# Kernel tuning notes

Measured on AMD Instinct MI355X. Metric: run time of the kernel, lower is better.

Reference implementation:

```python
import jax, jax.numpy as jnp
import numpy as np

E, S, G, H, O = 50000, 16, 64, 256, 16


def _mlp(x, W0, b0, W1, b1, W2, b2):
    # x: [..., 2] -> [..., out]
    x = jax.nn.relu(x @ W0 + b0)
    x = jax.nn.relu(x @ W1 + b1)
    return x @ W2 + b2


def setup_inputs() -> dict:
    key = jax.random.key(0)
    ks = jax.random.split(key, 9)
    ob = jax.random.normal(ks[0], (E, S, 3), dtype=jnp.float32)
    action = jax.random.randint(ks[1], (E, S), 0, O).astype(jnp.int64)
    graph_ids = jnp.sort(jax.random.randint(ks[2], (E,), 0, G)).astype(jnp.int32)
    def lin(k, fin, fout):
        return jax.random.normal(k, (fin, fout), dtype=jnp.float32) / jnp.sqrt(jnp.float32(fin))
    return {
        "ob": ob, "action": action, "graph_ids": graph_ids,
        "aW0": lin(ks[3], 2, H), "ab0": jnp.zeros((H,), jnp.float32),
        "aW1": lin(ks[4], H, H), "ab1": jnp.zeros((H,), jnp.float32),
        "aW2": lin(ks[5], H, O), "ab2": jnp.zeros((O,), jnp.float32),
        "cW0": lin(ks[6], 2, H), "cb0": jnp.zeros((H,), jnp.float32),
        "cW1": lin(ks[7], H, H), "cb1": jnp.zeros((H,), jnp.float32),
        "cW2": lin(ks[8], H, 1), "cb2": jnp.zeros((1,), jnp.float32),
    }


def reference(ob, action, graph_ids, aW0, ab0, aW1, ab1, aW2, ab2,
              cW0, cb0, cW1, cb1, cW2, cb2):
    num_edges = ob.shape[0]
    # edge_mask: torch `ob.select(2,0).long() == 0` (truncation toward zero)
    edge_mask = ob[..., 0].astype(jnp.int32) == 0            # [E,S] bool
    mf = edge_mask.astype(ob.dtype)                          # [E,S]
    h = ob[..., 1:3]                                         # [E,S,2]

    # Actor logits over all (edge,sample); mask replaces gather/scatter
    logits = _mlp(h, aW0, ab0, aW1, ab1, aW2, ab2)           # [E,S,O]
    logp = jax.nn.log_softmax(logits, axis=-1)               # [E,S,O]

    # log-prob of given actions, scattered to zeros outside the mask
    alp = jnp.take_along_axis(logp, action[..., None], axis=-1)[..., 0]
    action_log_probs = alp * mf                              # [E,S]

    # critic edge values, scattered to zeros outside the mask
    vals = _mlp(h, cW0, cb0, cW1, cb1, cW2, cb2)[..., 0] * mf  # [E,S]

    # entropy averaged over masked (subgraph) entries only
    ent = -jnp.sum(jnp.exp(logp) * logp, axis=-1)            # [E,S]
    avg_entropy = jnp.sum(ent * mf) / jnp.sum(mf)

    # sum_efeat: per-graph segment sum over edges, divided by num_edges
    value_preds = jax.ops.segment_sum(vals, graph_ids, num_segments=G) / num_edges  # [G,S]

    return action_log_probs, avg_entropy, value_preds, edge_mask
```

## Files before the change

### kernel.cpp

```cpp
#include <hip/hip_runtime.h>
#include <stdint.h>


typedef __attribute__((ext_vector_type(8))) short bf16x8;
typedef __attribute__((ext_vector_type(4))) float f32x4;
typedef __attribute__((ext_vector_type(4))) uint32_t u32x4;

#define NROWS    800000
#define NCHUNK   12500
#define OUT_ENT  800000
#define OUT_VP   800001
#define OUT_MASK 801025

#define SWZ(row) ((((row) & 7) << 4) ^ (((row) & 16) << 1))

__device__ __forceinline__ short f2bf(float x) {
  union { float f; uint32_t u; } v; v.f = x;
  return (short)(uint16_t)((v.u + 0x7FFFu + ((v.u >> 16) & 1u)) >> 16);
}
__device__ __forceinline__ float bf2f(short h) {
  union { uint32_t u; float f; } v; v.u = ((uint32_t)(uint16_t)h) << 16;
  return v.f;
}
template <int C>
__device__ __forceinline__ float dppf(float x) {
  int r = __builtin_amdgcn_update_dpp(0, __builtin_bit_cast(int, x), C, 0xF, 0xF, true);
  return __builtin_bit_cast(float, r);
}
__device__ __forceinline__ float red16_sum(float x) {
  x += dppf<0xB1>(x); x += dppf<0x4E>(x); x += dppf<0x124>(x); x += dppf<0x128>(x); return x;
}
__device__ __forceinline__ float red16_max(float x) {
  x = fmaxf(x, dppf<0xB1>(x)); x = fmaxf(x, dppf<0x4E>(x));
  x = fmaxf(x, dppf<0x124>(x)); x = fmaxf(x, dppf<0x128>(x)); return x;
}
__device__ __forceinline__ uint32_t cvt_pk_bf16(float a, float b) {
  uint32_t r; asm("v_cvt_pk_bf16_f32 %0, %1, %2" : "=v"(r) : "v"(a), "v"(b)); return r;
}

__global__ void zero_kernel(float* out, float* wsf) {
  int t = threadIdx.x + blockIdx.x * blockDim.x;
  for (int i = t; i < 1025; i += 1024) out[OUT_ENT + i] = 0.0f;
  if (t == 0) { wsf[0] = 0.0f; wsf[1] = 0.0f; }
}
__global__ void final_kernel(float* out, const float* wsf) {
  if (threadIdx.x == 0 && blockIdx.x == 0)
    out[OUT_ENT] = (wsf[1] > 0.0f) ? (wsf[0] / wsf[1]) : 0.0f;
}

#define A_ACT1 0
#define A_ACT2 32768
#define A_W2H  65536
#define A_W0   73728
#define A_B0   75776
#define A_OB   76800
#define A_SZ   78848

__global__ void __launch_bounds__(512, 2) ac_actor(
    const float* __restrict__ ob, const int* __restrict__ action,
    const float* __restrict__ aW0, const float* __restrict__ ab0,
    const float* __restrict__ aW1, const float* __restrict__ ab1,
    const float* __restrict__ aW2, const float* __restrict__ ab2,
    float* __restrict__ out, float* __restrict__ wsf)
{
  extern __shared__ char smem[];
  float* w0buf = (float*)(smem + A_W0);
  float* b0buf = (float*)(smem + A_B0);
  float* obufA = (float*)(smem + A_OB);
  const f32x4* w04 = (const f32x4*)(smem + A_W0);
  const f32x4* b04 = (const f32x4*)(smem + A_B0);
  __shared__ float went[8], wmf[8];

  const int tid = threadIdx.x, lane = tid & 63, wave = tid >> 6;
  const int l15 = lane & 15, l4 = lane >> 4;

  w0buf[tid] = aW0[tid];
  if (tid < 256) b0buf[tid] = ab0[tid];
  for (int id = tid; id < 4096; id += 512) {
    int n = id >> 8, k = id & 255;
    *(short*)(smem + A_W2H + n * 512 + ((k * 2) ^ SWZ(n))) = f2bf(aW2[k * 16 + n]);
  }
  const int colbase = wave * 32;
  float b1lane[2] = { ab1[colbase + l15], ab1[colbase + 16 + l15] };
  float b2lane = ab2[l15];
  bf16x8 bh[2][8];
  #pragma unroll
  for (int ct = 0; ct < 2; ++ct) {
    const int n = colbase + ct * 16 + l15;
    #pragma unroll
    for (int ks = 0; ks < 8; ++ks) {
      const int k0 = ks * 32 + 8 * l4;
      bf16x8 h8;
      #pragma unroll
      for (int j = 0; j < 8; ++j) h8[j] = f2bf(aW1[(k0 + j) * 256 + n]);
      bh[ct][ks] = h8;
    }
  }
  const int c0 = blockIdx.x, stride = gridDim.x;
  float sob = 0.0f;
  if (tid < 192) { obufA[tid] = ob[c0 * 192 + tid]; }
  { int cn = c0 + stride; if (cn < NCHUNK && tid < 192) sob = ob[cn * 192 + tid]; }
  __syncthreads();

  float entacc = 0.0f, mfacc = 0.0f;
  int buf = 0;
  for (int c = c0; c < NCHUNK; c += stride, buf ^= 1) {
    const int row0 = c * 64;
    const float* ocur = obufA + buf * 256;
    float* onxt = (float*)(obufA + (buf ^ 1) * 256);

    if (tid < 64) out[OUT_MASK + row0 + tid] = ((int)ocur[tid * 3] == 0) ? 1.0f : 0.0f;
    {
      const int kb = tid & 31;
      f32x4 wa0 = w04[kb * 2], wa1 = w04[kb * 2 + 1];
      f32x4 wb0 = w04[64 + kb * 2], wb1 = w04[64 + kb * 2 + 1];
      f32x4 ba0 = b04[kb * 2], ba1 = b04[kb * 2 + 1];
      #pragma unroll
      for (int i = 0; i < 4; ++i) {
        int row = wave * 2 + 16 * i + (lane >> 5);
        float h0 = ocur[row * 3 + 1], h1 = ocur[row * 3 + 2];
        f32x4 va, vb;
        #pragma unroll
        for (int j = 0; j < 4; ++j) {
          va[j] = fmaxf(fmaf(h0, wa0[j], fmaf(h1, wb0[j], ba0[j])), 0.0f);
          vb[j] = fmaxf(fmaf(h0, wa1[j], fmaf(h1, wb1[j], ba1[j])), 0.0f);
        }
        u32x4 v;
        v[0] = cvt_pk_bf16(va[0], va[1]);
        v[1] = cvt_pk_bf16(va[2], va[3]);
        v[2] = cvt_pk_bf16(vb[0], vb[1]);
        v[3] = cvt_pk_bf16(vb[2], vb[3]);
        *(u32x4*)(smem + A_ACT1 + row * 512 + ((kb * 16) ^ SWZ(row))) = v;
      }
    }
    if (tid < 192) onxt[tid] = sob;
    { int c2 = c + 2 * stride; if (c2 < NCHUNK && tid < 192) sob = ob[c2 * 192 + tid]; }
    __syncthreads();

    const bool evn = (l15 & 1) == 0;
    #pragma unroll 1
    for (int rtp = 0; rtp < 2; ++rtp) {
      f32x4 acc[2][2];
      #pragma unroll
      for (int h = 0; h < 2; ++h)
        #pragma unroll
        for (int ct = 0; ct < 2; ++ct) acc[h][ct] = (f32x4){0.f, 0.f, 0.f, 0.f};
      const int rA0 = rtp * 32 + l15, rA1 = rA0 + 16;
      #pragma unroll
      for (int ks = 0; ks < 8; ++ks) {
        const int cb = ks * 64 + 16 * l4;
        bf16x8 a0 = *(const bf16x8*)(smem + A_ACT1 + rA0 * 512 + (cb ^ SWZ(rA0)));
        bf16x8 a1 = *(const bf16x8*)(smem + A_ACT1 + rA1 * 512 + (cb ^ SWZ(rA1)));
        acc[0][0] = __builtin_amdgcn_mfma_f32_16x16x32_bf16(a0, bh[0][ks], acc[0][0], 0, 0, 0);
        acc[0][1] = __builtin_amdgcn_mfma_f32_16x16x32_bf16(a0, bh[1][ks], acc[0][1], 0, 0, 0);
        acc[1][0] = __builtin_amdgcn_mfma_f32_16x16x32_bf16(a1, bh[0][ks], acc[1][0], 0, 0, 0);
        acc[1][1] = __builtin_amdgcn_mfma_f32_16x16x32_bf16(a1, bh[1][ks], acc[1][1], 0, 0, 0);
      }
      #pragma unroll
      for (int ct = 0; ct < 2; ++ct) {
        const int colb = (colbase + ct * 16 + (l15 & ~1)) * 2;
        #pragma unroll
        for (int r = 0; r < 4; ++r) {
          float v0 = fmaxf(acc[0][ct][r] + b1lane[ct], 0.0f);
          float v1 = fmaxf(acc[1][ct][r] + b1lane[ct], 0.0f);
          float n0 = dppf<0xB1>(v0), n1 = dppf<0xB1>(v1);
          uint32_t w = cvt_pk_bf16(evn ? v0 : n1, evn ? n0 : v1);
          int rr = rtp * 32 + (evn ? 0 : 16) + 4 * l4 + r;
          *(uint32_t*)(smem + A_ACT2 + rr * 512 + (colb ^ SWZ(rr))) = w;
        }
      }
    }
    __syncthreads();

    if (wave < 4) {
      const int rowA = wave * 16 + l15;
      const int swA = SWZ(rowA), swW = SWZ(l15);
      f32x4 ae = {0.f,0.f,0.f,0.f}, ao = {0.f,0.f,0.f,0.f};
      #pragma unroll
      for (int ks = 0; ks < 8; ks += 2) {
        const int cb0 = ks * 64 + 16 * l4, cb1 = cb0 + 64;
        bf16x8 a0 = *(const bf16x8*)(smem + A_ACT2 + rowA * 512 + (cb0 ^ swA));
        bf16x8 a1 = *(const bf16x8*)(smem + A_ACT2 + rowA * 512 + (cb1 ^ swA));
        bf16x8 w0f = *(const bf16x8*)(smem + A_W2H + l15 * 512 + (cb0 ^ swW));
        bf16x8 w1f = *(const bf16x8*)(smem + A_W2H + l15 * 512 + (cb1 ^ swW));
        ae = __builtin_amdgcn_mfma_f32_16x16x32_bf16(a0, w0f, ae, 0, 0, 0);
        ao = __builtin_amdgcn_mfma_f32_16x16x32_bf16(a1, w1f, ao, 0, 0, 0);
      }
      #pragma unroll
      for (int r = 0; r < 4; ++r) {
        const int rl = wave * 16 + 4 * l4 + r;
        float x = ae[r] + ao[r] + b2lane;
        float m = red16_max(x);
        float e = __expf(x - m);
        float s = red16_sum(e);
        float t = red16_sum(e * (x - m));
        float ls = __logf(s);
        float mfr = ((int)ob[(row0 + rl) * 3] == 0) ? 1.0f : 0.0f;
        int av = action[row0 + rl];
        if (l15 == av) out[row0 + rl] = (x - m - ls) * mfr;
        if (l15 == 0) { entacc += (ls - t / s) * mfr; mfacc += mfr; }
      }
    }
  }
  #pragma unroll
  for (int d = 1; d < 64; d <<= 1) { entacc += __shfl_xor(entacc, d); mfacc += __shfl_xor(mfacc, d); }
  if (lane == 0) { went[wave] = entacc; wmf[wave] = mfacc; }
  __syncthreads();
  if (tid == 0) {
    float e = 0.f, m = 0.f;
    #pragma unroll
    for (int i = 0; i < 8; ++i) { e += went[i]; m += wmf[i]; }
    atomicAdd(&wsf[0], e); atomicAdd(&wsf[1], m);
  }
}

#define C_ACT1 0
#define C_ACT2 32768
#define C_W0   65536
#define C_B0   67584
#define C_W2F  68608
#define C_OB   69632
#define C_SZ   71680

__global__ void __launch_bounds__(512, 2) ac_critic(
    const float* __restrict__ ob, const int* __restrict__ graph_ids,
    const float* __restrict__ cW0, const float* __restrict__ cb0,
    const float* __restrict__ cW1, const float* __restrict__ cb1,
    const float* __restrict__ cW2, const float* __restrict__ cb2,
    float* __restrict__ out)
{
  extern __shared__ char smem[];
  float* w0buf = (float*)(smem + C_W0);
  float* b0buf = (float*)(smem + C_B0);
  float* w2buf = (float*)(smem + C_W2F);
  float* obufA = (float*)(smem + C_OB);
  const f32x4* w04 = (const f32x4*)(smem + C_W0);
  const f32x4* b04 = (const f32x4*)(smem + C_B0);
  const f32x4* w24 = (const f32x4*)(smem + C_W2F);

  const int tid = threadIdx.x, lane = tid & 63, wave = tid >> 6;
  const int l15 = lane & 15, l4 = lane >> 4;

  w0buf[tid] = cW0[tid];
  if (tid < 256) b0buf[tid] = cb0[tid];
  if (tid >= 256 && tid < 512) w2buf[tid - 256] = cW2[tid - 256];
  const float cb2v = cb2[0];
  const int colbase = wave * 32;
  float b1lane[2] = { cb1[colbase + l15], cb1[colbase + 16 + l15] };

  bf16x8 bh[2][8];
  #pragma unroll
  for (int ct = 0; ct < 2; ++ct) {
    const int n = colbase + ct * 16 + l15;
    #pragma unroll
    for (int ks = 0; ks < 8; ++ks) {
      const int k0 = ks * 32 + 8 * l4;
      bf16x8 h8;
      #pragma unroll
      for (int j = 0; j < 8; ++j) h8[j] = f2bf(cW1[(k0 + j) * 256 + n]);
      bh[ct][ks] = h8;
    }
  }
  const int c0 = blockIdx.x, stride = gridDim.x;
  float sob = 0.0f;
  if (tid < 192) { obufA[tid] = ob[c0 * 192 + tid]; }
  { int cn = c0 + stride; if (cn < NCHUNK && tid < 192) sob = ob[cn * 192 + tid]; }
  __syncthreads();

  int buf = 0;
  for (int c = c0; c < NCHUNK; c += stride, buf ^= 1) {
    const int row0 = c * 64;
    const float* ocur = obufA + buf * 256;
    float* onxt = (float*)(obufA + (buf ^ 1) * 256);

    {
      const int kb = tid & 31;
      f32x4 wa0 = w04[kb * 2], wa1 = w04[kb * 2 + 1];
      f32x4 wb0 = w04[64 + kb * 2], wb1 = w04[64 + kb * 2 + 1];
      f32x4 ba0 = b04[kb * 2], ba1 = b04[kb * 2 + 1];
      #pragma unroll
      for (int i = 0; i < 4; ++i) {
        int row = wave * 2 + 16 * i + (lane >> 5);
        float h0 = ocur[row * 3 + 1], h1 = ocur[row * 3 + 2];
        f32x4 va, vb;
        #pragma unroll
        for (int j = 0; j < 4; ++j) {
          va[j] = fmaxf(fmaf(h0, wa0[j], fmaf(h1, wb0[j], ba0[j])), 0.0f);
          vb[j] = fmaxf(fmaf(h0, wa1[j], fmaf(h1, wb1[j], ba1[j])), 0.0f);
        }
        u32x4 v;
        v[0] = cvt_pk_bf16(va[0], va[1]);
        v[1] = cvt_pk_bf16(va[2], va[3]);
        v[2] = cvt_pk_bf16(vb[0], vb[1]);
        v[3] = cvt_pk_bf16(vb[2], vb[3]);
        *(u32x4*)(smem + C_ACT1 + row * 512 + ((kb * 16) ^ SWZ(row))) = v;
      }
    }
    if (tid < 192) onxt[tid] = sob;
    { int c2 = c + 2 * stride; if (c2 < NCHUNK && tid < 192) sob = ob[c2 * 192 + tid]; }
    __syncthreads();

    const bool evn = (l15 & 1) == 0;
    #pragma unroll 1
    for (int rtp = 0; rtp < 2; ++rtp) {
      f32x4 acc[2][2];
      #pragma unroll
      for (int h = 0; h < 2; ++h)
        #pragma unroll
        for (int ct = 0; ct < 2; ++ct) acc[h][ct] = (f32x4){0.f, 0.f, 0.f, 0.f};
      const int rA0 = rtp * 32 + l15, rA1 = rA0 + 16;
      #pragma unroll
      for (int ks = 0; ks < 8; ++ks) {
        const int cb = ks * 64 + 16 * l4;
        bf16x8 a0 = *(const bf16x8*)(smem + C_ACT1 + rA0 * 512 + (cb ^ SWZ(rA0)));
        bf16x8 a1 = *(const bf16x8*)(smem + C_ACT1 + rA1 * 512 + (cb ^ SWZ(rA1)));
        acc[0][0] = __builtin_amdgcn_mfma_f32_16x16x32_bf16(a0, bh[0][ks], acc[0][0], 0, 0, 0);
        acc[0][1] = __builtin_amdgcn_mfma_f32_16x16x32_bf16(a0, bh[1][ks], acc[0][1], 0, 0, 0);
        acc[1][0] = __builtin_amdgcn_mfma_f32_16x16x32_bf16(a1, bh[0][ks], acc[1][0], 0, 0, 0);
        acc[1][1] = __builtin_amdgcn_mfma_f32_16x16x32_bf16(a1, bh[1][ks], acc[1][1], 0, 0, 0);
      }
      #pragma unroll
      for (int ct = 0; ct < 2; ++ct) {
        const int colb = (colbase + ct * 16 + (l15 & ~1)) * 2;
        #pragma unroll
        for (int r = 0; r < 4; ++r) {
          float v0 = fmaxf(acc[0][ct][r] + b1lane[ct], 0.0f);
          float v1 = fmaxf(acc[1][ct][r] + b1lane[ct], 0.0f);
          float n0 = dppf<0xB1>(v0), n1 = dppf<0xB1>(v1);
          uint32_t w = cvt_pk_bf16(evn ? v0 : n1, evn ? n0 : v1);
          int rr = rtp * 32 + (evn ? 0 : 16) + 4 * l4 + r;
          *(uint32_t*)(smem + C_ACT2 + rr * 512 + (colb ^ SWZ(rr))) = w;
        }
      }
    }
    __syncthreads();

    if (wave < 4) {
      const int rt = wave;
      const int row = rt * 16 + l15;
      const int sw = SWZ(row);
      float val = 0.0f;
      #pragma unroll
      for (int ks = 0; ks < 8; ++ks) {
        bf16x8 a = *(const bf16x8*)(smem + C_ACT2 + row * 512 + ((ks * 64 + 16 * l4) ^ sw));
        f32x4 wA = w24[ks * 8 + 2 * l4], wB = w24[ks * 8 + 2 * l4 + 1];
        #pragma unroll
        for (int j = 0; j < 4; ++j) {
          val = fmaf(bf2f(a[j]), wA[j], val);
          val = fmaf(bf2f(a[4 + j]), wB[j], val);
        }
      }
      val += __shfl_xor(val, 16);
      val += __shfl_xor(val, 32);
      if (l4 == 0) {
        float o0 = ob[(row0 + row) * 3];
        if ((int)o0 == 0) {
          int g = graph_ids[c * 4 + rt];
          atomicAdd(&out[OUT_VP + g * 16 + l15], (val + cb2v) * (1.0f / 50000.0f));
        }
      }
    }
  }
}

extern "C" void kernel_launch(void* const* d_in, const int* in_sizes, int n_in,
                              void* d_out, int out_size, void* d_ws, size_t ws_size,
                              hipStream_t stream) {
  const float* ob     = (const float*)d_in[0];
  const int*   action = (const int*)d_in[1];
  const int*   gids   = (const int*)d_in[2];
  const float* aW0 = (const float*)d_in[3],  *ab0 = (const float*)d_in[4];
  const float* aW1 = (const float*)d_in[5],  *ab1 = (const float*)d_in[6];
  const float* aW2 = (const float*)d_in[7],  *ab2 = (const float*)d_in[8];
  const float* cW0 = (const float*)d_in[9],  *cb0 = (const float*)d_in[10];
  const float* cW1 = (const float*)d_in[11], *cb1 = (const float*)d_in[12];
  const float* cW2 = (const float*)d_in[13], *cb2 = (const float*)d_in[14];
  float* out = (float*)d_out;
  float* wsf = (float*)d_ws;

  zero_kernel<<<2, 512, 0, stream>>>(out, wsf);
  ac_actor<<<512, 512, A_SZ, stream>>>(ob, action, aW0, ab0, aW1, ab1, aW2, ab2, out, wsf);
  ac_critic<<<512, 512, C_SZ, stream>>>(ob, gids, cW0, cb0, cW1, cb1, cW2, cb2, out);
  final_kernel<<<1, 64, 0, stream>>>(out, wsf);
}
```

Measured before the change: 483.5 us.

## Fuse critic output layer into layer-2 epilogue via cross-lane reduction

The critic's final 256→1 projection is now applied in the layer-2 MFMA epilogue. Each lane multiplies its ReLU outputs by per-column cW2 weights held in registers, reduces across 16 lanes, and writes per-wave partial sums to a small LDS buffer. Wave 0 then sums the 8 partials per row and does the masked atomic. This removes the bf16 ACT2 LDS round trip and the 4-wave dot-product pass, cuts LDS use, and reads the mask from the staged ob buffer instead of global memory. In exchange it adds shuffle reductions in every wave and serializes the final sum onto wave 0.

```diff
diff --git a/kernel.cpp b/kernel.cpp
--- a/kernel.cpp
+++ b/kernel.cpp
@@ -215,12 +215,11 @@
 }
 
 #define C_ACT1 0
-#define C_ACT2 32768
-#define C_W0   65536
-#define C_B0   67584
-#define C_W2F  68608
-#define C_OB   69632
-#define C_SZ   71680
+#define C_W0   32768
+#define C_B0   34816
+#define C_OB   35840
+#define C_VB   37888
+#define C_SZ   39936
 
 __global__ void __launch_bounds__(512, 2) ac_critic(
     const float* __restrict__ ob, const int* __restrict__ graph_ids,
@@ -232,21 +231,21 @@
   extern __shared__ char smem[];
   float* w0buf = (float*)(smem + C_W0);
   float* b0buf = (float*)(smem + C_B0);
-  float* w2buf = (float*)(smem + C_W2F);
   float* obufA = (float*)(smem + C_OB);
+  float* vbuf  = (float*)(smem + C_VB);
   const f32x4* w04 = (const f32x4*)(smem + C_W0);
   const f32x4* b04 = (const f32x4*)(smem + C_B0);
-  const f32x4* w24 = (const f32x4*)(smem + C_W2F);
 
   const int tid = threadIdx.x, lane = tid & 63, wave = tid >> 6;
   const int l15 = lane & 15, l4 = lane >> 4;
 
   w0buf[tid] = cW0[tid];
   if (tid < 256) b0buf[tid] = cb0[tid];
-  if (tid >= 256 && tid < 512) w2buf[tid - 256] = cW2[tid - 256];
   const float cb2v = cb2[0];
   const int colbase = wave * 32;
   float b1lane[2] = { cb1[colbase + l15], cb1[colbase + 16 + l15] };
+  const float w2c0 = cW2[colbase + l15];
+  const float w2c1 = cW2[colbase + 16 + l15];
 
   bf16x8 bh[2][8];
   #pragma unroll
@@ -269,7 +268,6 @@
 
   int buf = 0;
   for (int c = c0; c < NCHUNK; c += stride, buf ^= 1) {
-    const int row0 = c * 64;
     const float* ocur = obufA + buf * 256;
     float* onxt = (float*)(obufA + (buf ^ 1) * 256);
 
@@ -300,7 +298,9 @@
     { int c2 = c + 2 * stride; if (c2 < NCHUNK && tid < 192) sob = ob[c2 * 192 + tid]; }
     __syncthreads();
 
-    const bool evn = (l15 & 1) == 0;
+    float o0w0 = 0.0f;
+    if (wave == 0) o0w0 = ocur[lane * 3];
+
     #pragma unroll 1
     for (int rtp = 0; rtp < 2; ++rtp) {
       f32x4 acc[2][2];
@@ -320,44 +320,25 @@
         acc[1][1] = __builtin_amdgcn_mfma_f32_16x16x32_bf16(a1, bh[1][ks], acc[1][1], 0, 0, 0);
       }
       #pragma unroll
-      for (int ct = 0; ct < 2; ++ct) {
-        const int colb = (colbase + ct * 16 + (l15 & ~1)) * 2;
+      for (int h = 0; h < 2; ++h) {
         #pragma unroll
         for (int r = 0; r < 4; ++r) {
-          float v0 = fmaxf(acc[0][ct][r] + b1lane[ct], 0.0f);
-          float v1 = fmaxf(acc[1][ct][r] + b1lane[ct], 0.0f);
-          float n0 = dppf<0xB1>(v0), n1 = dppf<0xB1>(v1);
-          uint32_t w = cvt_pk_bf16(evn ? v0 : n1, evn ? n0 : v1);
-          int rr = rtp * 32 + (evn ? 0 : 16) + 4 * l4 + r;
-          *(uint32_t*)(smem + C_ACT2 + rr * 512 + (colb ^ SWZ(rr))) = w;
+          float p = fmaxf(acc[h][0][r] + b1lane[0], 0.0f) * w2c0
+                  + fmaxf(acc[h][1][r] + b1lane[1], 0.0f) * w2c1;
+          p = red16_sum(p);
+          if (l15 == 0) vbuf[wave * 64 + rtp * 32 + h * 16 + 4 * l4 + r] = p;
         }
       }
     }
     __syncthreads();
 
-    if (wave < 4) {
-      const int rt = wave;
-      const int row = rt * 16 + l15;
-      const int sw = SWZ(row);
-      float val = 0.0f;
-      #pragma unroll
-      for (int ks = 0; ks < 8; ++ks) {
-        bf16x8 a = *(const bf16x8*)(smem + C_ACT2 + row * 512 + ((ks * 64 + 16 * l4) ^ sw));
-        f32x4 wA = w24[ks * 8 + 2 * l4], wB = w24[ks * 8 + 2 * l4 + 1];
-        #pragma unroll
-        for (int j = 0; j < 4; ++j) {
-          val = fmaf(bf2f(a[j]), wA[j], val);
-          val = fmaf(bf2f(a[4 + j]), wB[j], val);
-        }
-      }
-      val += __shfl_xor(val, 16);
-      val += __shfl_xor(val, 32);
-      if (l4 == 0) {
-        float o0 = ob[(row0 + row) * 3];
-        if ((int)o0 == 0) {
-          int g = graph_ids[c * 4 + rt];
-          atomicAdd(&out[OUT_VP + g * 16 + l15], (val + cb2v) * (1.0f / 50000.0f));
-        }
+    if (wave == 0) {
+      float v = 0.0f;
+      #pragma unroll
+      for (int w = 0; w < 8; ++w) v += vbuf[w * 64 + lane];
+      if ((int)o0w0 == 0) {
+        int g = graph_ids[c * 4 + (lane >> 4)];
+        atomicAdd(&out[OUT_VP + g * 16 + (lane & 15)], (v + cb2v) * (1.0f / 50000.0f));
       }
     }
   }
```

New measurement: 502.6 us. 3.9% more time.
